# Optimization experiments

Hardware: AMD Instinct MI355X
Metric: run time of the kernel (lower is better)

The kernel has to match this reference:

```python
import jax, jax.numpy as jnp
import numpy as np
import math

WINDOW = 2048
EMBED = 1024
BATCH = 8


def setup_inputs() -> dict:
    key = jax.random.key(0)
    ks = jax.random.split(key, 7)
    s = 1.0 / math.sqrt(EMBED)
    return {
        "embeddings": jax.random.normal(ks[0], (BATCH, WINDOW, EMBED), dtype=jnp.float32),
        "Wq": jax.random.uniform(ks[1], (EMBED, EMBED), jnp.float32, -s, s),
        "bq": jax.random.uniform(ks[2], (EMBED,), jnp.float32, -s, s),
        "Wk": jax.random.uniform(ks[3], (EMBED, EMBED), jnp.float32, -s, s),
        "bk": jax.random.uniform(ks[4], (EMBED,), jnp.float32, -s, s),
        "Wv": jax.random.uniform(ks[5], (EMBED, EMBED), jnp.float32, -s, s),
        "bv": jax.random.uniform(ks[6], (EMBED,), jnp.float32, -s, s),
    }


def reference(embeddings, Wq, bq, Wk, bk, Wv, bv):
    # Linear layers: x @ W.T + b (torch nn.Linear convention)
    Q = jnp.einsum('bse,fe->bsf', embeddings, Wq) + bq
    K = jnp.einsum('bse,fe->bsf', embeddings, Wk) + bk
    V = jnp.einsum('bse,fe->bsf', embeddings, Wv) + bv
    scale = 1.0 / math.sqrt(EMBED)
    # [B, S, S] score matrix: A[b, i, j] = Q_i . K_j / sqrt(d)
    A = jnp.einsum('bie,bje->bij', Q, K) * scale
    # causal additive mask: -inf where j > i (strictly upper triangular)
    mask = jnp.triu(jnp.full((WINDOW, WINDOW), -jnp.inf, dtype=A.dtype), k=1)
    A = A + mask
    # NOTE: faithful to original nn.Softmax(dim=1): normalize over QUERY axis
    P = jax.nn.softmax(A, axis=1)
    return jnp.einsum('bij,bje->bie', P, V)
```

## Files before the change

kernel.cpp:

```cpp
#include <hip/hip_runtime.h>
#include <stdint.h>

#define WINDOW 2048
#define EMBED  1024
#define BATCH  8
#define MTOT   (BATCH*WINDOW)

typedef unsigned short u16;
typedef __bf16 bf16x8 __attribute__((ext_vector_type(8)));
typedef float  f32x4  __attribute__((ext_vector_type(4)));

#define BK 64
#define KSCALE 0.04508422717564447f

#define BM2 256
#define BN2 256
#define HALF2 8192
#define PLD  260

#define WAITVM4 asm volatile("s_waitcnt vmcnt(4)" ::: "memory")
#define WAITVM0 asm volatile("s_waitcnt vmcnt(0)" ::: "memory")
#define SBAR    __builtin_amdgcn_s_barrier()

__device__ __forceinline__ u16 f2bf(float f) {
  union { float f; unsigned u; } a; a.f = f;
  unsigned r = a.u + 0x7FFF + ((a.u >> 16) & 1);
  return (u16)(r >> 16);
}
__device__ __forceinline__ float bf2f(u16 u) {
  union { unsigned u; float f; } a; a.u = ((unsigned)u) << 16;
  return a.f;
}

__device__ __forceinline__ void gload16(const u16* g, u16* l) {
  __builtin_amdgcn_global_load_lds(
      (const __attribute__((address_space(1))) unsigned int*)g,
      (__attribute__((address_space(3))) unsigned int*)l, 16, 0, 0);
}


__device__ __forceinline__ void gemm256(
    const u16* __restrict__ A, int lda,
    const u16* __restrict__ B, int ldb,
    int nt, u16* lds, f32x4 acc[8][4])
{
  const int tid  = threadIdx.x;
  const int lane = tid & 63;
  const int wid  = tid >> 6;
  const int wm   = (wid >> 2) * 128;
  const int wn   = (wid & 3) * 64;
  const int lrow = lane & 15;
  const int hi   = lane >> 4;
  u16* dA = lds;
  u16* dB = lds + 4 * HALF2;

  int aoff[8], boff[4];
  #pragma unroll
  for (int mi = 0; mi < 8; ++mi) {
    int r = wm + mi * 16 + lrow;
    aoff[mi] = r * 32 + ((hi ^ ((r >> 1) & 3)) << 3);
  }
  #pragma unroll
  for (int ni = 0; ni < 4; ++ni) {
    int r = wn + ni * 16 + lrow;
    boff[ni] = r * 32 + ((hi ^ ((r >> 1) & 3)) << 3);
  }

  const int f0 = tid, f1 = 512 + tid;
  const int r0 = f0 >> 2, r1 = f1 >> 2;
  const int c0 = (((f0 & 3) ^ ((r0 >> 1) & 3)) << 3);
  const int c1 = (((f1 & 3) ^ ((r1 >> 1) & 3)) << 3);
  const u16* pA0 = A + (size_t)r0 * lda + c0;
  const u16* pA1 = A + (size_t)r1 * lda + c1;
  const u16* pB0 = B + (size_t)r0 * ldb + c0;
  const u16* pB1 = B + (size_t)r1 * ldb + c1;
  const int d0 = f0 * 8, d1 = f1 * 8;

  gload16(pA0,      dA + d0);         gload16(pA1,      dA + d1);
  gload16(pB0,      dB + d0);         gload16(pB1,      dB + d1);
  gload16(pA0 + 32, dA + HALF2 + d0); gload16(pA1 + 32, dA + HALF2 + d1);
  gload16(pB0 + 32, dB + HALF2 + d0); gload16(pB1 + 32, dB + HALF2 + d1);
  pA0 += BK; pA1 += BK; pB0 += BK; pB1 += BK;
  WAITVM4;
  SBAR;

  for (int t = 0; t < nt; ++t) {
    const int cb = (t & 1) * 2;
    const int nb = ((t + 1) & 1) * 2;
    u16* LA0 = dA + cb * HALF2;  u16* LA1 = LA0 + HALF2;
    u16* LB0 = dB + cb * HALF2;  u16* LB1 = LB0 + HALF2;
    const bool s = (t + 1) < nt;
    bf16x8 av[8], bv[4];

    #pragma unroll
    for (int mi = 0; mi < 8; ++mi) av[mi] = *(const bf16x8*)(LA0 + aoff[mi]);
    #pragma unroll
    for (int ni = 0; ni < 4; ++ni) bv[ni] = *(const bf16x8*)(LB0 + boff[ni]);
    if (s) {
      gload16(pA0, dA + nb * HALF2 + d0); gload16(pA1, dA + nb * HALF2 + d1);
      gload16(pB0, dB + nb * HALF2 + d0); gload16(pB1, dB + nb * HALF2 + d1);
    }
    __builtin_amdgcn_s_setprio(1);
    #pragma unroll
    for (int mi = 0; mi < 8; ++mi)
      #pragma unroll
      for (int ni = 0; ni < 4; ++ni)
        acc[mi][ni] = __builtin_amdgcn_mfma_f32_16x16x32_bf16(av[mi], bv[ni], acc[mi][ni], 0, 0, 0);
    __builtin_amdgcn_s_setprio(0);
    if (s) { WAITVM4; } else { WAITVM0; }
    SBAR;

    #pragma unroll
    for (int mi = 0; mi < 8; ++mi) av[mi] = *(const bf16x8*)(LA1 + aoff[mi]);
    #pragma unroll
    for (int ni = 0; ni < 4; ++ni) bv[ni] = *(const bf16x8*)(LB1 + boff[ni]);
    if (s) {
      gload16(pA0 + 32, dA + nb * HALF2 + HALF2 + d0); gload16(pA1 + 32, dA + nb * HALF2 + HALF2 + d1);
      gload16(pB0 + 32, dB + nb * HALF2 + HALF2 + d0); gload16(pB1 + 32, dB + nb * HALF2 + HALF2 + d1);
      pA0 += BK; pA1 += BK; pB0 += BK; pB1 += BK;
    }
    __builtin_amdgcn_s_setprio(1);
    #pragma unroll
    for (int mi = 0; mi < 8; ++mi)
      #pragma unroll
      for (int ni = 0; ni < 4; ++ni)
        acc[mi][ni] = __builtin_amdgcn_mfma_f32_16x16x32_bf16(av[mi], bv[ni], acc[mi][ni], 0, 0, 0);
    __builtin_amdgcn_s_setprio(0);
    if (s) { WAITVM4; }
    SBAR;
  }
}

__global__ __launch_bounds__(256) void k_cvt(const float* __restrict__ in,
                                             u16* __restrict__ out, int n) {
  int i = (blockIdx.x * 256 + threadIdx.x) * 4;
  if (i >= n) return;
  float4 v = *(const float4*)(in + i);
  ushort4 o;
  o.x = f2bf(v.x); o.y = f2bf(v.y); o.z = f2bf(v.z); o.w = f2bf(v.w);
  *(ushort4*)(out + i) = o;
}

__global__ __launch_bounds__(256) void k_cvtw(const float* __restrict__ w0,
                                              const float* __restrict__ w1,
                                              const float* __restrict__ w2,
                                              u16* __restrict__ out) {
  const float* in = (blockIdx.y == 0) ? w0 : (blockIdx.y == 1) ? w1 : w2;
  u16* o = out + (size_t)blockIdx.y * EMBED * EMBED;
  int i = (blockIdx.x * 256 + threadIdx.x) * 4;
  float4 v = *(const float4*)(in + i);
  ushort4 r;
  r.x = f2bf(v.x); r.y = f2bf(v.y); r.z = f2bf(v.z); r.w = f2bf(v.w);
  *(ushort4*)(o + i) = r;
}

__global__ __launch_bounds__(512, 2) void k_qkv(
    const u16* __restrict__ Xb, const u16* __restrict__ Wb,
    const float* __restrict__ bq, const float* __restrict__ bk, const float* __restrict__ bv,
    u16* __restrict__ Q, u16* __restrict__ Ks, u16* __restrict__ V)
{
  __shared__ u16 lds[8 * HALF2];
  const int m0 = blockIdx.x * BM2;
  const int n0 = blockIdx.y * BN2;
  const int z  = blockIdx.z;
  const u16*   W    = Wb + (size_t)z * EMBED * EMBED;
  const float* bias = (z == 0) ? bq : (z == 1) ? bk : bv;
  u16* out          = (z == 0) ? Q  : (z == 1) ? Ks : V;
  const float scale = (z == 1) ? KSCALE : 1.0f;

  f32x4 acc[8][4];
  const f32x4 zz = {0.f,0.f,0.f,0.f};
  #pragma unroll
  for (int i = 0; i < 8; ++i) for (int j = 0; j < 4; ++j) acc[i][j] = zz;
  gemm256(Xb + (size_t)m0 * EMBED, EMBED, W + (size_t)n0 * EMBED, EMBED,
          EMBED / BK, lds, acc);

  const int lane = threadIdx.x & 63, wid = threadIdx.x >> 6;
  const int wm = (wid >> 2) * 128, wn = (wid & 3) * 64;
  const int lrow = lane & 15, hi = lane >> 4;
  #pragma unroll
  for (int mi = 0; mi < 8; ++mi)
    #pragma unroll
    for (int ni = 0; ni < 4; ++ni)
      #pragma unroll
      for (int rr = 0; rr < 4; ++rr) {
        int gm = m0 + wm + mi * 16 + hi * 4 + rr;
        int gn = n0 + wn + ni * 16 + lrow;
        out[(size_t)gm * EMBED + gn] = f2bf((acc[mi][ni][rr] + bias[gn]) * scale);
      }
}

__global__ __launch_bounds__(512, 2) void k_spd(
    const u16* __restrict__ Q, const u16* __restrict__ Ks,
    u16* __restrict__ P, float* __restrict__ D)
{
  const int i0 = blockIdx.x * BM2;
  const int j0 = blockIdx.y * BN2;
  if (j0 > i0) return;
  const int b  = blockIdx.z;
  __shared__ u16 lds[BM2 * PLD];
  const u16* A = Q  + (size_t)b * WINDOW * EMBED + (size_t)i0 * EMBED;
  const u16* B = Ks + (size_t)b * WINDOW * EMBED + (size_t)j0 * EMBED;
  f32x4 acc[8][4];
  const f32x4 zz = {0.f,0.f,0.f,0.f};
  #pragma unroll
  for (int i = 0; i < 8; ++i) for (int j = 0; j < 4; ++j) acc[i][j] = zz;
  gemm256(A, EMBED, B, EMBED, EMBED / BK, lds, acc);

  u16* Pb   = P + (size_t)b * WINDOW * WINDOW;
  float* Db = D + (size_t)b * WINDOW;
  const int tid  = threadIdx.x;
  const int lane = tid & 63, wid = tid >> 6;
  const int wm = (wid >> 2) * 128, wn = (wid & 3) * 64;
  const int lrow = lane & 15, hi = lane >> 4;

  #pragma unroll
  for (int ni = 0; ni < 4; ++ni) {
    int lj = wn + ni * 16 + lrow;
    float csum = 0.f;
    #pragma unroll
    for (int mi = 0; mi < 8; ++mi)
      #pragma unroll
      for (int rr = 0; rr < 4; ++rr) {
        int li = wm + mi * 16 + hi * 4 + rr;
        float p = ((i0 + li) >= (j0 + lj)) ? exp2f(acc[mi][ni][rr]) : 0.0f;
        lds[li * PLD + lj] = f2bf(p);
        csum += p;
      }
    csum += __shfl_xor(csum, 16, 64);
    csum += __shfl_xor(csum, 32, 64);
    if (hi == 0) atomicAdd(&Db[j0 + lj], csum);
  }
  __syncthreads();

  #pragma unroll
  for (int it = 0; it < 16; ++it) {
    int f   = it * 512 + tid;
    int row = f >> 5;
    int c   = f & 31;
    bf16x8 v = *(const bf16x8*)(lds + row * PLD + c * 8);
    *(bf16x8*)(Pb + (size_t)(i0 + row) * WINDOW + j0 + c * 8) = v;
  }
}

__global__ __launch_bounds__(256) void k_vdt(
    const u16* __restrict__ V, const float* __restrict__ D, u16* __restrict__ Vdt)
{
  __shared__ u16 tile[64][68];
  const int j0 = blockIdx.x * 64, e0 = blockIdx.y * 64, b = blockIdx.z;
  const u16* Vb = V   + (size_t)b * WINDOW * EMBED;
  u16* Tb       = Vdt + (size_t)b * EMBED * WINDOW;
  const float* Db = D + (size_t)b * WINDOW;
  const int t = threadIdx.x;
  const int rr = t >> 4;
  const int cc = (t & 15) * 4;
  #pragma unroll
  for (int p = 0; p < 4; ++p) {
    int r = p * 16 + rr;
    *(uint2*)&tile[r][cc] = *(const uint2*)(Vb + (size_t)(j0 + r) * EMBED + e0 + cc);
  }
  __syncthreads();
  #pragma unroll
  for (int p = 0; p < 4; ++p) {
    int er = p * 16 + rr;
    ushort4 o;
    o.x = f2bf(bf2f(tile[cc + 0][er]) / Db[j0 + cc + 0]);
    o.y = f2bf(bf2f(tile[cc + 1][er]) / Db[j0 + cc + 1]);
    o.z = f2bf(bf2f(tile[cc + 2][er]) / Db[j0 + cc + 2]);
    o.w = f2bf(bf2f(tile[cc + 3][er]) / Db[j0 + cc + 3]);
    *(ushort4*)(Tb + (size_t)(e0 + er) * WINDOW + j0 + cc) = o;
  }
}

__global__ __launch_bounds__(512, 2) void k_out(
    const u16* __restrict__ P, const u16* __restrict__ Vdt, float* __restrict__ O)
{
  __shared__ u16 lds[8 * HALF2];
  const int i0 = ((int)gridDim.x - 1 - (int)blockIdx.x) * BM2;
  const int e0 = blockIdx.y * BN2;
  const int b  = blockIdx.z;
  const u16* A = P   + (size_t)b * WINDOW * WINDOW + (size_t)i0 * WINDOW;
  const u16* B = Vdt + (size_t)b * EMBED * WINDOW  + (size_t)e0 * WINDOW;
  f32x4 acc[8][4];
  const f32x4 zz = {0.f,0.f,0.f,0.f};
  #pragma unroll
  for (int i = 0; i < 8; ++i) for (int j = 0; j < 4; ++j) acc[i][j] = zz;
  gemm256(A, WINDOW, B, WINDOW, (i0 + BM2) / BK, lds, acc);

  float* Ob = O + (size_t)b * WINDOW * EMBED;
  const int lane = threadIdx.x & 63, wid = threadIdx.x >> 6;
  const int wm = (wid >> 2) * 128, wn = (wid & 3) * 64;
  const int lrow = lane & 15, hi = lane >> 4;
  #pragma unroll
  for (int mi = 0; mi < 8; ++mi)
    #pragma unroll
    for (int ni = 0; ni < 4; ++ni)
      #pragma unroll
      for (int rr = 0; rr < 4; ++rr) {
        int gi = i0 + wm + mi * 16 + hi * 4 + rr;
        int ge = e0 + wn + ni * 16 + lrow;
        Ob[(size_t)gi * EMBED + ge] = acc[mi][ni][rr];
      }
}

extern "C" void kernel_launch(void* const* d_in, const int* in_sizes, int n_in,
                              void* d_out, int out_size, void* d_ws, size_t ws_size,
                              hipStream_t stream) {
  const float* X  = (const float*)d_in[0];
  const float* Wq = (const float*)d_in[1];
  const float* bq = (const float*)d_in[2];
  const float* Wk = (const float*)d_in[3];
  const float* bk = (const float*)d_in[4];
  const float* Wv = (const float*)d_in[5];
  const float* bv = (const float*)d_in[6];
  float* O = (float*)d_out;

  char* ws = (char*)d_ws;
  size_t off = 0;
  auto alloc = [&](size_t bytes) -> void* {
    void* p = ws + off; off += (bytes + 255) & ~(size_t)255; return p;
  };
  u16*  Xb  = (u16*)alloc((size_t)MTOT * EMBED * 2);
  u16*  Wb  = (u16*)alloc((size_t)3 * EMBED * EMBED * 2);
  u16*  Qb  = (u16*)alloc((size_t)MTOT * EMBED * 2);
  u16*  Kb  = (u16*)alloc((size_t)MTOT * EMBED * 2);
  u16*  Vb  = (u16*)alloc((size_t)MTOT * EMBED * 2);
  u16*  Vdt = (u16*)alloc((size_t)BATCH * EMBED * WINDOW * 2);
  u16*  P   = (u16*)alloc((size_t)BATCH * WINDOW * WINDOW * 2);
  float* D  = (float*)alloc((size_t)MTOT * 4);
  (void)ws_size; (void)in_sizes; (void)n_in; (void)out_size;

  k_cvt<<<dim3((MTOT * EMBED / 4 + 255) / 256), 256, 0, stream>>>(X, Xb, MTOT * EMBED);
  k_cvtw<<<dim3(EMBED * EMBED / 4 / 256, 3), 256, 0, stream>>>(Wq, Wk, Wv, Wb);

  k_qkv<<<dim3(MTOT / BM2, EMBED / BN2, 3), 512, 0, stream>>>(Xb, Wb, bq, bk, bv, Qb, Kb, Vb);

  (void)hipMemsetAsync(D, 0, (size_t)MTOT * 4, stream);
  k_spd<<<dim3(WINDOW / BM2, WINDOW / BN2, BATCH), 512, 0, stream>>>(Qb, Kb, P, D);

  k_vdt<<<dim3(WINDOW / 64, EMBED / 64, BATCH), 256, 0, stream>>>(Vb, D, Vdt);

  k_out<<<dim3(WINDOW / BM2, EMBED / BN2, BATCH), 512, 0, stream>>>(P, Vdt, O);
}
```

Measured before the change: 296.8 us.

## Remap score and output grids to triangular, XCD-aware 1D block schedules

k_spd now launches only the 288 lower-triangular tiles instead of 512 blocks with half exiting early. The tile index is decoded from a flat block id, and batches are rotated across XCDs so each chiplet's L2 sees a balanced mix of work. k_out likewise switches to a 1D grid that orders heavy rows first and places them on XCDs in a batch-rotated way to balance load and locality. This removes empty-block launch overhead and targets better L2 reuse and load balance, at the cost of a small index-decode loop per block.

```diff
diff --git a/kernel.cpp b/kernel.cpp
--- a/kernel.cpp
+++ b/kernel.cpp
@@ -194,10 +194,16 @@
     const u16* __restrict__ Q, const u16* __restrict__ Ks,
     u16* __restrict__ P, float* __restrict__ D)
 {
-  const int i0 = blockIdx.x * BM2;
-  const int j0 = blockIdx.y * BN2;
-  if (j0 > i0) return;
-  const int b  = blockIdx.z;
+  const int s   = blockIdx.x;
+  const int xcd = s & 7;
+  const int q   = s >> 3;
+  int it = 0;
+  while (q >= ((it + 1) * (it + 2)) / 2) ++it;
+  const int jt = q - (it * (it + 1)) / 2;
+  const int b  = (xcd - it) & 7;
+  const int i0 = it * BM2;
+  const int j0 = jt * BN2;
+
   __shared__ u16 lds[BM2 * PLD];
   const u16* A = Q  + (size_t)b * WINDOW * EMBED + (size_t)i0 * EMBED;
   const u16* B = Ks + (size_t)b * WINDOW * EMBED + (size_t)j0 * EMBED;
@@ -234,8 +240,8 @@
   __syncthreads();
 
   #pragma unroll
-  for (int it = 0; it < 16; ++it) {
-    int f   = it * 512 + tid;
+  for (int it2 = 0; it2 < 16; ++it2) {
+    int f   = it2 * 512 + tid;
     int row = f >> 5;
     int c   = f & 31;
     bf16x8 v = *(const bf16x8*)(lds + row * PLD + c * 8);
@@ -276,9 +282,15 @@
     const u16* __restrict__ P, const u16* __restrict__ Vdt, float* __restrict__ O)
 {
   __shared__ u16 lds[8 * HALF2];
-  const int i0 = ((int)gridDim.x - 1 - (int)blockIdx.x) * BM2;
-  const int e0 = blockIdx.y * BN2;
-  const int b  = blockIdx.z;
+  const int s   = blockIdx.x;
+  const int xcd = s & 7;
+  const int q   = s >> 3;
+  const int et  = q & 3;
+  const int it  = 7 - (q >> 2);
+  const int b   = (xcd - it) & 7;
+  const int i0  = it * BM2;
+  const int e0  = et * BN2;
+
   const u16* A = P   + (size_t)b * WINDOW * WINDOW + (size_t)i0 * WINDOW;
   const u16* B = Vdt + (size_t)b * EMBED * WINDOW  + (size_t)e0 * WINDOW;
   f32x4 acc[8][4];
@@ -336,9 +348,9 @@
   k_qkv<<<dim3(MTOT / BM2, EMBED / BN2, 3), 512, 0, stream>>>(Xb, Wb, bq, bk, bv, Qb, Kb, Vb);
 
   (void)hipMemsetAsync(D, 0, (size_t)MTOT * 4, stream);
-  k_spd<<<dim3(WINDOW / BM2, WINDOW / BN2, BATCH), 512, 0, stream>>>(Qb, Kb, P, D);
+  k_spd<<<dim3(288), 512, 0, stream>>>(Qb, Kb, P, D);
 
   k_vdt<<<dim3(WINDOW / 64, EMBED / 64, BATCH), 256, 0, stream>>>(Vb, D, Vdt);
 
-  k_out<<<dim3(WINDOW / BM2, EMBED / BN2, BATCH), 512, 0, stream>>>(P, Vdt, O);
-}
+  k_out<<<dim3(256), 512, 0, stream>>>(P, Vdt, O);
+}
```

Result: faster. 281.9 us, median of 2 (-5.0%).
